# Performance work log

Measured on AMD Instinct MI355X. Metric: run time of the kernel, lower is better.

## Reference

```python
import jax, jax.numpy as jnp
import numpy as np
import math

B, S, D, H = 4, 2048, 1024, 16
HD = D // H  # head_dim = 64


def setup_inputs() -> dict:
    key = jax.random.key(0)
    ks = jax.random.split(key, 12)
    inv = 1.0 / math.sqrt(D)
    inp = {
        "query": jax.random.normal(ks[0], (B, S, D), dtype=jnp.float32),
        "key": jax.random.normal(ks[1], (B, S, D), dtype=jnp.float32),
        "value": jax.random.normal(ks[2], (B, S, D), dtype=jnp.float32),
        # causal mask, broadcast over heads; guarantees no all-masked softmax rows
        "mask": jnp.tril(jnp.ones((S, S), dtype=jnp.int32))[None, None].repeat(B, axis=0),
        # linear params stored as (in, out); y = x @ W + b (same math as torch Linear)
        "Wq": jax.random.uniform(ks[3], (D, D), jnp.float32, -inv, inv),
        "bq": jax.random.uniform(ks[4], (D,), jnp.float32, -inv, inv),
        "Wk": jax.random.uniform(ks[5], (D, D), jnp.float32, -inv, inv),
        "bk": jax.random.uniform(ks[6], (D,), jnp.float32, -inv, inv),
        "Wv": jax.random.uniform(ks[7], (D, D), jnp.float32, -inv, inv),
        "bv": jax.random.uniform(ks[8], (D,), jnp.float32, -inv, inv),
        "Wo": jax.random.uniform(ks[9], (D, D), jnp.float32, -inv, inv),
        "bo": jax.random.uniform(ks[10], (D,), jnp.float32, -inv, inv),
    }
    return inp


def _split_heads(x):
    # [B, S, D] -> [B, H, S, HD]
    b, s, _ = x.shape
    return x.reshape(b, s, H, HD).transpose(0, 2, 1, 3)


def reference(query, key, value, mask, Wq, bq, Wk, bk, Wv, bv, Wo, bo):
    q = _split_heads(query @ Wq + bq)   # [B,H,S,HD]
    k = _split_heads(key @ Wk + bk)
    v = _split_heads(value @ Wv + bv)
    scores = jnp.einsum("bhqd,bhkd->bhqk", q, k)          # [B,H,S,S]
    scores = jnp.where(mask == 0, -jnp.inf, scores)
    attn = jax.nn.softmax(scores / math.sqrt(HD), axis=-1)
    attn = attn * mask.astype(attn.dtype)                  # post-softmax re-mask (as in source)
    out = jnp.einsum("bhqk,bhkd->bhqd", attn, v)           # [B,H,S,HD]
    out = out.transpose(0, 2, 1, 3).reshape(query.shape[0], -1, D)
    return out @ Wo + bo
```

## Files before the change

### kernel.cpp

```cpp
#include <hip/hip_runtime.h>

typedef __attribute__((ext_vector_type(8))) short short8;
typedef __attribute__((ext_vector_type(8))) unsigned short ushort8;
typedef __attribute__((ext_vector_type(4))) unsigned short us4;
typedef __attribute__((ext_vector_type(4))) float f32x4;
typedef __attribute__((ext_vector_type(4))) int i32x4;

#define S_LEN 2048
#define D_MODEL 1024
#define N_HEADS 16
#define HEAD_DIM 64

__device__ __forceinline__ unsigned short f2bf(float f) {
  union { float f; unsigned u; } x; x.f = f;
  unsigned r = x.u + 0x7FFFu + ((x.u >> 16) & 1u);
  return (unsigned short)(r >> 16);
}

__device__ __forceinline__ int pkbf(float a, float b) {
  union { float f; unsigned u; } x, y;
  x.f = a; y.f = b;
  return (int)__builtin_amdgcn_perm(y.u + 0x8000u, x.u + 0x8000u, 0x07060302u);
}

__global__ __launch_bounds__(256) void cvt3_kernel(const float* __restrict__ a,
                                                   const float* __restrict__ b,
                                                   const float* __restrict__ c,
                                                   unsigned short* __restrict__ oa,
                                                   unsigned short* __restrict__ ob,
                                                   unsigned short* __restrict__ oc) {
  int bid = blockIdx.x;
  const float* in = (bid < 4096) ? a : (bid < 8192 ? b : c);
  unsigned short* out = (bid < 4096) ? oa : (bid < 8192 ? ob : oc);
  int i = (bid & 4095) * 256 + threadIdx.x;
  const f32x4* in4 = (const f32x4*)in;
  f32x4 x = in4[2 * i], y = in4[2 * i + 1];
  i32x4 o;
  o[0] = pkbf(x[0], x[1]);
  o[1] = pkbf(x[2], x[3]);
  o[2] = pkbf(y[0], y[1]);
  o[3] = pkbf(y[2], y[3]);
  ((i32x4*)out)[i] = o;
}

__global__ __launch_bounds__(256) void transpose_w4(
    const float* __restrict__ Wq, const float* __restrict__ Wk,
    const float* __restrict__ Wv, const float* __restrict__ Wo,
    unsigned short* __restrict__ wqkvT, unsigned short* __restrict__ woT) {
  __shared__ float tile[64][65];
  const int z = blockIdx.z;
  const float* W = (z == 0) ? Wq : (z == 1) ? Wk : (z == 2) ? Wv : Wo;
  unsigned short* Wt = (z < 3) ? (wqkvT + (size_t)z * D_MODEL * D_MODEL) : woT;
  const int no = blockIdx.x * 64, ko = blockIdx.y * 64;
  const int tx = threadIdx.x & 63, ty = threadIdx.x >> 6;
  for (int r = ty; r < 64; r += 4)
    tile[r][tx] = W[(size_t)(ko + r) * D_MODEL + no + tx];
  __syncthreads();
  for (int r = ty; r < 64; r += 4)
    Wt[(size_t)(no + r) * D_MODEL + ko + tx] = f2bf(tile[tx][r]);
}

template <int MODE>
__global__ __launch_bounds__(256, 3) void proj_gemm(
    const unsigned short* __restrict__ A0,
    const unsigned short* __restrict__ A1,
    const unsigned short* __restrict__ A2,
    const unsigned short* __restrict__ Bt,
    const float* __restrict__ b0p, const float* __restrict__ b1p,
    const float* __restrict__ b2p,
    void* __restrict__ o0, void* __restrict__ o1, void* __restrict__ o2,
    float qscale) {
  extern __shared__ __align__(16) unsigned short smem_d[];
  const int tid = threadIdx.x;
  const int wave = tid >> 6, lane = tid & 63;
  const int quad = lane >> 4, l16 = lane & 15;

  const int nlin = blockIdx.y * (MODE == 0 ? 24 : 8) + blockIdx.x;
  const int xcd = nlin & 7;
  const int j = nlin >> 3;
  int bx_eff, by_eff;
  if (MODE == 0) {
    const int sel_i = j >> 6;
    const int rem = j & 63;
    by_eff = xcd * 8 + (rem >> 3);
    bx_eff = sel_i * 8 + (rem & 7);
  } else {
    by_eff = xcd * 8 + (j >> 3);
    bx_eff = j & 7;
  }
  const int m0 = by_eff * 128, n0 = bx_eff * 128;
  const int wm = (wave >> 1) * 64, wn = (wave & 1) * 64;

  const int sel = (MODE == 0) ? (n0 >> 10) : 0;
  const unsigned short* A = (MODE == 0) ? (sel == 0 ? A0 : sel == 1 ? A1 : A2) : A0;
  const float* bias = (MODE == 0) ? (sel == 0 ? b0p : sel == 1 ? b1p : b2p) : b0p;
  const float scale = (MODE == 0 && sel == 0) ? qscale : 1.0f;
  const int nb = (MODE == 0) ? (n0 & 1023) : n0;

  f32x4 acc[4][4] = {};

  const int lrow = lane >> 2;
  const int kcs = ((lane & 3) ^ ((lane >> 3) & 3)) << 3;

  auto stage = [&](int kt, int bsel) {
    unsigned short* Ab = smem_d + bsel * 8192;
    unsigned short* Bb = Ab + 4096;
    const int k0 = kt * 32;
#pragma unroll
    for (int c = 0; c < 2; ++c) {
      const int r = wave * 32 + c * 16;
      const unsigned short* ga = A + (size_t)(m0 + r + lrow) * D_MODEL + k0 + kcs;
      __builtin_amdgcn_global_load_lds((const __attribute__((address_space(1))) void*)ga,
          (__attribute__((address_space(3))) void*)(Ab + r * 32), 16, 0, 0);
      const unsigned short* gb = Bt + (size_t)(n0 + r + lrow) * D_MODEL + k0 + kcs;
      __builtin_amdgcn_global_load_lds((const __attribute__((address_space(1))) void*)gb,
          (__attribute__((address_space(3))) void*)(Bb + r * 32), 16, 0, 0);
    }
  };

  const int fsw = (quad ^ ((l16 >> 1) & 3)) << 3;

  auto preload = [&](short8* af, short8* bf, int bsel) {
    const unsigned short* Ab = smem_d + bsel * 8192;
    const unsigned short* Bb = Ab + 4096;
#pragma unroll
    for (int i = 0; i < 4; ++i)
      af[i] = *(const short8*)(Ab + (wm + i * 16 + l16) * 32 + fsw);
#pragma unroll
    for (int i = 0; i < 4; ++i)
      bf[i] = *(const short8*)(Bb + (wn + i * 16 + l16) * 32 + fsw);
  };

  auto mfma16 = [&](const short8* af, const short8* bf) {
#pragma unroll
    for (int i = 0; i < 4; ++i)
#pragma unroll
      for (int j2 = 0; j2 < 4; ++j2)
        acc[i][j2] = __builtin_amdgcn_mfma_f32_16x16x32_bf16(af[i], bf[j2], acc[i][j2], 0, 0, 0);
  };

  short8 afA[4], bfA[4], afB[4], bfB[4];

  stage(0, 0); stage(1, 1); stage(2, 2);
  asm volatile("s_waitcnt vmcnt(8)" ::: "memory");
  __builtin_amdgcn_s_barrier();
  __builtin_amdgcn_sched_barrier(0);
  preload(afA, bfA, 0);
  asm volatile("s_waitcnt lgkmcnt(0)" ::: "memory");
  asm volatile("s_waitcnt vmcnt(4)" ::: "memory");
  __builtin_amdgcn_s_barrier();
  __builtin_amdgcn_sched_barrier(0);

  int c0 = 0, c1 = 1, c2 = 2;
  for (int kt = 0; kt < 32; kt += 2) {
    preload(afB, bfB, c1);
    if (kt + 3 < 32) stage(kt + 3, c0);
    __builtin_amdgcn_sched_barrier(0);
    __builtin_amdgcn_s_setprio(1);
    mfma16(afA, bfA);
    __builtin_amdgcn_s_setprio(0);
    __builtin_amdgcn_sched_barrier(0);
    asm volatile("s_waitcnt lgkmcnt(0)" ::: "memory");
    if (kt + 3 < 32) { asm volatile("s_waitcnt vmcnt(4)" ::: "memory"); }
    else             { asm volatile("s_waitcnt vmcnt(0)" ::: "memory"); }
    __builtin_amdgcn_s_barrier();
    __builtin_amdgcn_sched_barrier(0);

    if (kt + 2 < 32) preload(afA, bfA, c2);
    if (kt + 4 < 32) stage(kt + 4, c1);
    __builtin_amdgcn_sched_barrier(0);
    __builtin_amdgcn_s_setprio(1);
    mfma16(afB, bfB);
    __builtin_amdgcn_s_setprio(0);
    __builtin_amdgcn_sched_barrier(0);
    asm volatile("s_waitcnt lgkmcnt(0)" ::: "memory");
    if (kt + 4 < 32)      { asm volatile("s_waitcnt vmcnt(4)" ::: "memory"); }
    else if (kt + 3 < 32) { asm volatile("s_waitcnt vmcnt(0)" ::: "memory"); }
    __builtin_amdgcn_s_barrier();
    __builtin_amdgcn_sched_barrier(0);

    int t0 = c0, t1 = c1;
    c0 = c2; c1 = t0; c2 = t1;
  }

  float bv4[4];
#pragma unroll
  for (int j2 = 0; j2 < 4; ++j2) bv4[j2] = bias[nb + wn + j2 * 16 + l16];

  if (MODE == 0) {
    if (sel < 2) {
      unsigned short* T = smem_d + wave * 1152;
      unsigned short* out = (unsigned short*)(sel == 0 ? o0 : o1);
      const int h = (nb + wn) >> 6;
#pragma unroll
      for (int i = 0; i < 4; ++i) {
#pragma unroll
        for (int j2 = 0; j2 < 4; ++j2)
#pragma unroll
          for (int r = 0; r < 4; ++r)
            T[(quad * 4 + r) * 72 + j2 * 16 + l16] = f2bf((acc[i][j2][r] + bv4[j2]) * scale);
        int m = m0 + wm + i * 16 + l16;
        int b = m >> 11, s = m & 2047;
#pragma unroll
        for (int t = 0; t < 2; ++t) {
          short8 row = *(const short8*)(T + l16 * 72 + t * 32 + quad * 8);
          *(short8*)(out + (((size_t)(b * N_HEADS + h) * S_LEN + s) << 6) + t * 32 + quad * 8) = row;
        }
      }
    } else {
      unsigned short* vt = (unsigned short*)o2;
#pragma unroll
      for (int i = 0; i < 4; ++i) {
        int m = m0 + wm + i * 16 + quad * 4;
        int b = m >> 11, s = m & 2047;
#pragma unroll
        for (int j2 = 0; j2 < 4; ++j2) {
          int n = nb + wn + j2 * 16 + l16;
          int h = n >> 6, d = n & 63;
          us4 pv;
#pragma unroll
          for (int r = 0; r < 4; ++r) pv[r] = f2bf(acc[i][j2][r] + bv4[j2]);
          *(us4*)(vt + (((size_t)(b * N_HEADS + h) * 64 + d) << 11) + s) = pv;
        }
      }
    }
  } else {
    float* Tf = (float*)smem_d + wave * 1088;
    float* out = (float*)o0;
#pragma unroll
    for (int i = 0; i < 4; ++i) {
#pragma unroll
      for (int j2 = 0; j2 < 4; ++j2)
#pragma unroll
        for (int r = 0; r < 4; ++r)
          Tf[(quad * 4 + r) * 68 + j2 * 16 + l16] = acc[i][j2][r] + bv4[j2];
      int m = m0 + wm + i * 16 + l16;
#pragma unroll
      for (int t = 0; t < 4; ++t) {
        f32x4 row = *(const f32x4*)(Tf + l16 * 68 + t * 16 + quad * 4);
        *(f32x4*)(out + (size_t)m * D_MODEL + nb + wn + t * 16 + quad * 4) = row;
      }
    }
  }
}

__global__ __launch_bounds__(256, 4) void flash_attn(
    const unsigned short* __restrict__ Qh,
    const unsigned short* __restrict__ Kh,
    const unsigned short* __restrict__ Vt,
    unsigned short* __restrict__ ctx) {
  __shared__ __align__(16) unsigned short smem[16384];
  const int tid = threadIdx.x;
  const int wave = tid >> 6, lane = tid & 63;
  const int quad = lane >> 4, l16 = lane & 15;
  const int l7 = l16 & 7;

  const int nlin = blockIdx.y * 16 + blockIdx.x;
  const int xcd = nlin & 7;
  const int rr = nlin >> 3;
  const int bh = xcd * 8 + (rr & 7);
  const int qslot = rr >> 3;
  const int qa = qslot & 3, qb = qslot >> 2;
  const int qbase = qa + ((qb >> 1) << 2);
  const int qi = (qb & 1) ? (15 - qbase) : qbase;
  const int q0 = qi * 128;
  const int nk = 2 * qi + 2;
  const size_t hb = (size_t)bh * (S_LEN * HEAD_DIM);
  const int srow = lane >> 3;
  const int schunk = ((lane & 7) ^ srow) * 8;

  auto stage = [&](int kt, int buf) {
    unsigned short* Kb = smem + buf * 8192;
    unsigned short* Vb = smem + buf * 8192 + 4096;
#pragma unroll
    for (int c = 0; c < 2; ++c) {
      int row = wave * 16 + c * 8 + srow;
      const unsigned short* gk = Kh + hb + (size_t)(kt * 64 + row) * 64 + schunk;
      __builtin_amdgcn_global_load_lds((const __attribute__((address_space(1))) void*)gk,
          (__attribute__((address_space(3))) void*)(Kb + (wave * 16 + c * 8) * 64), 16, 0, 0);
      const unsigned short* gv = Vt + hb + (size_t)row * S_LEN + kt * 64 + schunk;
      __builtin_amdgcn_global_load_lds((const __attribute__((address_space(1))) void*)gv,
          (__attribute__((address_space(3))) void*)(Vb + (wave * 16 + c * 8) * 64), 16, 0, 0);
    }
  };

  stage(0, 0);

  short8 qf[2][2];
#pragma unroll
  for (int s = 0; s < 2; ++s)
#pragma unroll
    for (int t = 0; t < 2; ++t)
      qf[s][t] = *(const short8*)(Qh + hb +
          (size_t)(q0 + wave * 32 + s * 16 + l16) * 64 + t * 32 + quad * 8);

  f32x4 o[4][2] = {};
  float rsum[2] = {0.f, 0.f};

  for (int kt = 0; kt < nk; ++kt) {
    __syncthreads();
    if (kt + 1 < nk) stage(kt + 1, (kt + 1) & 1);
    const unsigned short* Kb = smem + (kt & 1) * 8192;
    const unsigned short* Vb = Kb + 4096;

    if (kt * 64 > q0 + wave * 32 + 31) continue;

    f32x4 sc[2][4];
    __builtin_amdgcn_s_setprio(1);
#pragma unroll
    for (int nt = 0; nt < 4; ++nt) {
      short8 k0 = *(const short8*)(Kb + (nt * 16 + l16) * 64 + ((quad ^ l7) << 3));
      short8 k1 = *(const short8*)(Kb + (nt * 16 + l16) * 64 + (((4 + quad) ^ l7) << 3));
#pragma unroll
      for (int s = 0; s < 2; ++s) {
        f32x4 z = {};
        z = __builtin_amdgcn_mfma_f32_16x16x32_bf16(k0, qf[s][0], z, 0, 0, 0);
        sc[s][nt] = __builtin_amdgcn_mfma_f32_16x16x32_bf16(k1, qf[s][1], z, 0, 0, 0);
      }
    }
    __builtin_amdgcn_s_setprio(0);
    if (kt >= 2 * qi) {
#pragma unroll
      for (int s = 0; s < 2; ++s) {
        int qg = q0 + wave * 32 + s * 16 + l16;
#pragma unroll
        for (int nt = 0; nt < 4; ++nt) {
          int kg = kt * 64 + nt * 16 + quad * 4;
#pragma unroll
          for (int r = 0; r < 4; ++r)
            if (kg + r > qg) sc[s][nt][r] = -1e30f;
        }
      }
    }

    union { int i[4]; short8 v; } pf[2][2];
#pragma unroll
    for (int s = 0; s < 2; ++s) {
      int pk[4][2];
#pragma unroll
      for (int nt = 0; nt < 4; ++nt) {
        float p0 = __builtin_amdgcn_exp2f(sc[s][nt][0]);
        float p1 = __builtin_amdgcn_exp2f(sc[s][nt][1]);
        float p2 = __builtin_amdgcn_exp2f(sc[s][nt][2]);
        float p3 = __builtin_amdgcn_exp2f(sc[s][nt][3]);
        rsum[s] += (p0 + p1) + (p2 + p3);
        pk[nt][0] = pkbf(p0, p1);
        pk[nt][1] = pkbf(p2, p3);
      }
#pragma unroll
      for (int t = 0; t < 2; ++t) {
        int A = pk[t * 2][0], C = pk[t * 2 + 1][0];
        int B2 = pk[t * 2][1], D = pk[t * 2 + 1][1];
        asm("v_permlane32_swap_b32 %0, %1" : "+v"(A), "+v"(C));
        asm("v_permlane16_swap_b32 %0, %1" : "+v"(A), "+v"(C));
        asm("v_permlane32_swap_b32 %0, %1" : "+v"(B2), "+v"(D));
        asm("v_permlane16_swap_b32 %0, %1" : "+v"(B2), "+v"(D));
        pf[s][t].i[0] = A;
        pf[s][t].i[1] = B2;
        pf[s][t].i[2] = C;
        pf[s][t].i[3] = D;
      }
    }

    __builtin_amdgcn_s_setprio(1);
#pragma unroll
    for (int ntd = 0; ntd < 4; ++ntd) {
      short8 v0 = *(const short8*)(Vb + (ntd * 16 + l16) * 64 + ((quad ^ l7) << 3));
      short8 v1 = *(const short8*)(Vb + (ntd * 16 + l16) * 64 + (((4 + quad) ^ l7) << 3));
#pragma unroll
      for (int s = 0; s < 2; ++s) {
        o[ntd][s] = __builtin_amdgcn_mfma_f32_16x16x32_bf16(v0, pf[s][0].v, o[ntd][s], 0, 0, 0);
        o[ntd][s] = __builtin_amdgcn_mfma_f32_16x16x32_bf16(v1, pf[s][1].v, o[ntd][s], 0, 0, 0);
      }
    }
    __builtin_amdgcn_s_setprio(0);
  }

#pragma unroll
  for (int s = 0; s < 2; ++s) {
    rsum[s] += __shfl_xor(rsum[s], 16, 64);
    rsum[s] += __shfl_xor(rsum[s], 32, 64);
  }

  __syncthreads();
  unsigned short* Os = smem;
#pragma unroll
  for (int s = 0; s < 2; ++s) {
    float invl = 1.0f / rsum[s];
#pragma unroll
    for (int ntd = 0; ntd < 4; ++ntd) {
      us4 pk4;
#pragma unroll
      for (int r = 0; r < 4; ++r) pk4[r] = f2bf(o[ntd][s][r] * invl);
      *(us4*)(Os + (wave * 32 + s * 16 + l16) * 72 + ntd * 16 + quad * 4) = pk4;
    }
  }
  __syncthreads();
  const int b = bh >> 4, h = bh & 15;
#pragma unroll
  for (int it = 0; it < 4; ++it) {
    int e = it * 256 + tid;
    int row = e >> 3, c = (e & 7) * 8;
    short8 vrow = *(const short8*)(Os + row * 72 + c);
    *(short8*)(ctx + (size_t)(b * S_LEN + q0 + row) * D_MODEL + h * HEAD_DIM + c) = vrow;
  }
}

extern "C" void kernel_launch(void* const* d_in, const int* in_sizes, int n_in,
                              void* d_out, int out_size, void* d_ws, size_t ws_size,
                              hipStream_t stream) {
  (void)in_sizes; (void)n_in; (void)out_size;
  const float* q  = (const float*)d_in[0];
  const float* k  = (const float*)d_in[1];
  const float* v  = (const float*)d_in[2];
  const float* Wq = (const float*)d_in[4];
  const float* bq = (const float*)d_in[5];
  const float* Wk = (const float*)d_in[6];
  const float* bk = (const float*)d_in[7];
  const float* Wv = (const float*)d_in[8];
  const float* bv = (const float*)d_in[9];
  const float* Wo = (const float*)d_in[10];
  const float* bo = (const float*)d_in[11];
  float* out = (float*)d_out;

  if (ws_size < 109051904u) return;
  char* ws = (char*)d_ws;
  unsigned short* xq    = (unsigned short*)(ws);
  unsigned short* xk    = (unsigned short*)(ws + 16777216);
  unsigned short* xv    = (unsigned short*)(ws + 33554432);
  unsigned short* wqkvT = (unsigned short*)(ws + 50331648);
  unsigned short* woT   = (unsigned short*)(ws + 56623104);
  unsigned short* qh    = (unsigned short*)(ws + 58720256);
  unsigned short* kh    = qh + 8388608;
  unsigned short* vt    = kh + 8388608;
  unsigned short* ctx   = xq;

  static int attr_done = 0;
  if (!attr_done) {
    auto* k0f = proj_gemm<0>;
    auto* k1f = proj_gemm<1>;
    hipFuncSetAttribute(reinterpret_cast<const void*>(k0f),
                        hipFuncAttributeMaxDynamicSharedMemorySize, 49152);
    hipFuncSetAttribute(reinterpret_cast<const void*>(k1f),
                        hipFuncAttributeMaxDynamicSharedMemorySize, 49152);
    attr_done = 1;
  }

  cvt3_kernel<<<12288, 256, 0, stream>>>(q, k, v, xq, xk, xv);
  transpose_w4<<<dim3(16, 16, 4), 256, 0, stream>>>(Wq, Wk, Wv, Wo, wqkvT, woT);
  proj_gemm<0><<<dim3(24, 64), 256, 49152, stream>>>(xq, xk, xv, wqkvT, bq, bk, bv,
                                                     qh, kh, vt, 0.125f * 1.44269504088896f);
  flash_attn<<<dim3(16, 64), 256, 0, stream>>>(qh, kh, vt, ctx);
  proj_gemm<1><<<dim3(8, 64), 256, 49152, stream>>>(ctx, ctx, ctx, woT, bo, bo, bo,
                                                    out, out, out, 1.0f);
}
```

Baseline: 334.2 us.

## Widen projection GEMM tiles to 128x256 with double-buffered LDS staging

Result: slower. 1.179 ms (+252.8%).

```diff
diff --git a/kernel.cpp b/kernel.cpp
--- a/kernel.cpp
+++ b/kernel.cpp
@@ -75,21 +75,15 @@
   const int wave = tid >> 6, lane = tid & 63;
   const int quad = lane >> 4, l16 = lane & 15;
 
-  const int nlin = blockIdx.y * (MODE == 0 ? 24 : 8) + blockIdx.x;
+  const int GX = (MODE == 0) ? 12 : 4;
+  const int nlin = blockIdx.y * GX + blockIdx.x;
   const int xcd = nlin & 7;
   const int j = nlin >> 3;
   int bx_eff, by_eff;
-  if (MODE == 0) {
-    const int sel_i = j >> 6;
-    const int rem = j & 63;
-    by_eff = xcd * 8 + (rem >> 3);
-    bx_eff = sel_i * 8 + (rem & 7);
-  } else {
-    by_eff = xcd * 8 + (j >> 3);
-    bx_eff = j & 7;
-  }
-  const int m0 = by_eff * 128, n0 = bx_eff * 128;
-  const int wm = (wave >> 1) * 64, wn = (wave & 1) * 64;
+  if (MODE == 0) { by_eff = xcd * 8 + j / 12; bx_eff = j % 12; }
+  else           { by_eff = xcd * 8 + (j >> 2); bx_eff = j & 3; }
+  const int m0 = by_eff * 128, n0 = bx_eff * 256;
+  const int wm = (wave >> 1) * 64, wn = (wave & 1) * 128;
 
   const int sel = (MODE == 0) ? (n0 >> 10) : 0;
   const unsigned short* A = (MODE == 0) ? (sel == 0 ? A0 : sel == 1 ? A1 : A2) : A0;
@@ -97,13 +91,13 @@
   const float scale = (MODE == 0 && sel == 0) ? qscale : 1.0f;
   const int nb = (MODE == 0) ? (n0 & 1023) : n0;
 
-  f32x4 acc[4][4] = {};
+  f32x4 acc[4][8] = {};
 
   const int lrow = lane >> 2;
   const int kcs = ((lane & 3) ^ ((lane >> 3) & 3)) << 3;
 
   auto stage = [&](int kt, int bsel) {
-    unsigned short* Ab = smem_d + bsel * 8192;
+    unsigned short* Ab = smem_d + bsel * 12288;
     unsigned short* Bb = Ab + 4096;
     const int k0 = kt * 32;
 #pragma unroll
@@ -112,6 +106,10 @@
       const unsigned short* ga = A + (size_t)(m0 + r + lrow) * D_MODEL + k0 + kcs;
       __builtin_amdgcn_global_load_lds((const __attribute__((address_space(1))) void*)ga,
           (__attribute__((address_space(3))) void*)(Ab + r * 32), 16, 0, 0);
+    }
+#pragma unroll
+    for (int c = 0; c < 4; ++c) {
+      const int r = wave * 64 + c * 16;
       const unsigned short* gb = Bt + (size_t)(n0 + r + lrow) * D_MODEL + k0 + kcs;
       __builtin_amdgcn_global_load_lds((const __attribute__((address_space(1))) void*)gb,
           (__attribute__((address_space(3))) void*)(Bb + r * 32), 16, 0, 0);
@@ -121,90 +119,86 @@
   const int fsw = (quad ^ ((l16 >> 1) & 3)) << 3;
 
   auto preload = [&](short8* af, short8* bf, int bsel) {
-    const unsigned short* Ab = smem_d + bsel * 8192;
+    const unsigned short* Ab = smem_d + bsel * 12288;
     const unsigned short* Bb = Ab + 4096;
 #pragma unroll
     for (int i = 0; i < 4; ++i)
       af[i] = *(const short8*)(Ab + (wm + i * 16 + l16) * 32 + fsw);
 #pragma unroll
+    for (int j2 = 0; j2 < 8; ++j2)
+      bf[j2] = *(const short8*)(Bb + (wn + j2 * 16 + l16) * 32 + fsw);
+  };
+
+  auto mfma32 = [&](const short8* af, const short8* bf) {
+#pragma unroll
     for (int i = 0; i < 4; ++i)
-      bf[i] = *(const short8*)(Bb + (wn + i * 16 + l16) * 32 + fsw);
-  };
-
-  auto mfma16 = [&](const short8* af, const short8* bf) {
-#pragma unroll
-    for (int i = 0; i < 4; ++i)
-#pragma unroll
-      for (int j2 = 0; j2 < 4; ++j2)
+#pragma unroll
+      for (int j2 = 0; j2 < 8; ++j2)
         acc[i][j2] = __builtin_amdgcn_mfma_f32_16x16x32_bf16(af[i], bf[j2], acc[i][j2], 0, 0, 0);
   };
 
-  short8 afA[4], bfA[4], afB[4], bfB[4];
-
-  stage(0, 0); stage(1, 1); stage(2, 2);
-  asm volatile("s_waitcnt vmcnt(8)" ::: "memory");
+  short8 afA[4], bfA[8], afB[4], bfB[8];
+
+  stage(0, 0); stage(1, 1);
+  asm volatile("s_waitcnt vmcnt(6)" ::: "memory");
   __builtin_amdgcn_s_barrier();
   __builtin_amdgcn_sched_barrier(0);
   preload(afA, bfA, 0);
   asm volatile("s_waitcnt lgkmcnt(0)" ::: "memory");
-  asm volatile("s_waitcnt vmcnt(4)" ::: "memory");
+  asm volatile("s_waitcnt vmcnt(0)" ::: "memory");
   __builtin_amdgcn_s_barrier();
   __builtin_amdgcn_sched_barrier(0);
 
-  int c0 = 0, c1 = 1, c2 = 2;
   for (int kt = 0; kt < 32; kt += 2) {
-    preload(afB, bfB, c1);
-    if (kt + 3 < 32) stage(kt + 3, c0);
+    preload(afB, bfB, 1);
+    if (kt + 2 < 32) stage(kt + 2, 0);
     __builtin_amdgcn_sched_barrier(0);
     __builtin_amdgcn_s_setprio(1);
-    mfma16(afA, bfA);
+    mfma32(afA, bfA);
     __builtin_amdgcn_s_setprio(0);
     __builtin_amdgcn_sched_barrier(0);
     asm volatile("s_waitcnt lgkmcnt(0)" ::: "memory");
-    if (kt + 3 < 32) { asm volatile("s_waitcnt vmcnt(4)" ::: "memory"); }
-    else             { asm volatile("s_waitcnt vmcnt(0)" ::: "memory"); }
+    asm volatile("s_waitcnt vmcnt(0)" ::: "memory");
     __builtin_amdgcn_s_barrier();
     __builtin_amdgcn_sched_barrier(0);
 
-    if (kt + 2 < 32) preload(afA, bfA, c2);
-    if (kt + 4 < 32) stage(kt + 4, c1);
+    if (kt + 2 < 32) preload(afA, bfA, 0);
+    if (kt + 3 < 32) stage(kt + 3, 1);
     __builtin_amdgcn_sched_barrier(0);
     __builtin_amdgcn_s_setprio(1);
-    mfma16(afB, bfB);
+    mfma32(afB, bfB);
     __builtin_amdgcn_s_setprio(0);
     __builtin_amdgcn_sched_barrier(0);
     asm volatile("s_waitcnt lgkmcnt(0)" ::: "memory");
-    if (kt + 4 < 32)      { asm volatile("s_waitcnt vmcnt(4)" ::: "memory"); }
-    else if (kt + 3 < 32) { asm volatile("s_waitcnt vmcnt(0)" ::: "memory"); }
+    asm volatile("s_waitcnt vmcnt(0)" ::: "memory");
     __builtin_amdgcn_s_barrier();
     __builtin_amdgcn_sched_barrier(0);
-
-    int t0 = c0, t1 = c1;
-    c0 = c2; c1 = t0; c2 = t1;
-  }
-
-  float bv4[4];
-#pragma unroll
-  for (int j2 = 0; j2 < 4; ++j2) bv4[j2] = bias[nb + wn + j2 * 16 + l16];
+  }
+
+  float bv8[8];
+#pragma unroll
+  for (int j2 = 0; j2 < 8; ++j2) bv8[j2] = bias[nb + wn + j2 * 16 + l16];
 
   if (MODE == 0) {
     if (sel < 2) {
-      unsigned short* T = smem_d + wave * 1152;
+      unsigned short* T = smem_d + wave * 2176;
       unsigned short* out = (unsigned short*)(sel == 0 ? o0 : o1);
-      const int h = (nb + wn) >> 6;
+      const int h0 = (nb + wn) >> 6;
 #pragma unroll
       for (int i = 0; i < 4; ++i) {
 #pragma unroll
-        for (int j2 = 0; j2 < 4; ++j2)
+        for (int j2 = 0; j2 < 8; ++j2)
 #pragma unroll
           for (int r = 0; r < 4; ++r)
-            T[(quad * 4 + r) * 72 + j2 * 16 + l16] = f2bf((acc[i][j2][r] + bv4[j2]) * scale);
+            T[(quad * 4 + r) * 136 + j2 * 16 + l16] = f2bf((acc[i][j2][r] + bv8[j2]) * scale);
         int m = m0 + wm + i * 16 + l16;
         int b = m >> 11, s = m & 2047;
 #pragma unroll
-        for (int t = 0; t < 2; ++t) {
-          short8 row = *(const short8*)(T + l16 * 72 + t * 32 + quad * 8);
-          *(short8*)(out + (((size_t)(b * N_HEADS + h) * S_LEN + s) << 6) + t * 32 + quad * 8) = row;
+        for (int t = 0; t < 4; ++t) {
+          short8 row = *(const short8*)(T + l16 * 136 + t * 32 + quad * 8);
+          int c = t * 32 + quad * 8;
+          int h = h0 + (c >> 6), d = c & 63;
+          *(short8*)(out + (((size_t)(b * N_HEADS + h) * S_LEN + s) << 6) + d) = row;
         }
       }
     } else {
@@ -214,30 +208,30 @@
         int m = m0 + wm + i * 16 + quad * 4;
         int b = m >> 11, s = m & 2047;
 #pragma unroll
-        for (int j2 = 0; j2 < 4; ++j2) {
+        for (int j2 = 0; j2 < 8; ++j2) {
           int n = nb + wn + j2 * 16 + l16;
           int h = n >> 6, d = n & 63;
           us4 pv;
 #pragma unroll
-          for (int r = 0; r < 4; ++r) pv[r] = f2bf(acc[i][j2][r] + bv4[j2]);
+          for (int r = 0; r < 4; ++r) pv[r] = f2bf(acc[i][j2][r] + bv8[j2]);
           *(us4*)(vt + (((size_t)(b * N_HEADS + h) * 64 + d) << 11) + s) = pv;
         }
       }
     }
   } else {
-    float* Tf = (float*)smem_d + wave * 1088;
+    float* Tf = (float*)smem_d + wave * 2176;
     float* out = (float*)o0;
 #pragma unroll
     for (int i = 0; i < 4; ++i) {
 #pragma unroll
-      for (int j2 = 0; j2 < 4; ++j2)
+      for (int j2 = 0; j2 < 8; ++j2)
 #pragma unroll
         for (int r = 0; r < 4; ++r)
-          Tf[(quad * 4 + r) * 68 + j2 * 16 + l16] = acc[i][j2][r] + bv4[j2];
+          Tf[(quad * 4 + r) * 136 + j2 * 16 + l16] = acc[i][j2][r] + bv8[j2];
       int m = m0 + wm + i * 16 + l16;
 #pragma unroll
-      for (int t = 0; t < 4; ++t) {
-        f32x4 row = *(const f32x4*)(Tf + l16 * 68 + t * 16 + quad * 4);
+      for (int t = 0; t < 8; ++t) {
+        f32x4 row = *(const f32x4*)(Tf + l16 * 136 + t * 16 + quad * 4);
         *(f32x4*)(out + (size_t)m * D_MODEL + nb + wn + t * 16 + quad * 4) = row;
       }
     }
@@ -448,9 +442,9 @@
 
   cvt3_kernel<<<12288, 256, 0, stream>>>(q, k, v, xq, xk, xv);
   transpose_w4<<<dim3(16, 16, 4), 256, 0, stream>>>(Wq, Wk, Wv, Wo, wqkvT, woT);
-  proj_gemm<0><<<dim3(24, 64), 256, 49152, stream>>>(xq, xk, xv, wqkvT, bq, bk, bv,
+  proj_gemm<0><<<dim3(12, 64), 256, 49152, stream>>>(xq, xk, xv, wqkvT, bq, bk, bv,
                                                      qh, kh, vt, 0.125f * 1.44269504088896f);
   flash_attn<<<dim3(16, 64), 256, 0, stream>>>(qh, kh, vt, ctx);
-  proj_gemm<1><<<dim3(8, 64), 256, 49152, stream>>>(ctx, ctx, ctx, woT, bo, bo, bo,
+  proj_gemm<1><<<dim3(4, 64), 256, 49152, stream>>>(ctx, ctx, ctx, woT, bo, bo, bo,
                                                     out, out, out, 1.0f);
 }
```
